# Kernel tuning notes

Hardware: AMD Instinct MI355X
Metric: run time of the kernel (lower is better)

Reference implementation:

```python
import jax, jax.numpy as jnp
import numpy as np

B, L, H, U = 4, 1024, 16, 64  # batch, length, num_heads, units (per-head dim)
D_IN = 1024                   # input feature dim
D_MODEL = H * U               # 1024


def setup_inputs() -> dict:
    key = jax.random.key(0)
    ks = jax.random.split(key, 12)
    s_in = 1.0 / np.sqrt(D_IN)
    s_md = 1.0 / np.sqrt(D_MODEL)
    return {
        "v": jax.random.normal(ks[0], (B, L, D_IN), jnp.float32),
        "k": jax.random.normal(ks[1], (B, L, D_IN), jnp.float32),
        "q": jax.random.normal(ks[2], (B, L, D_IN), jnp.float32),
        "wq": jax.random.normal(ks[3], (D_IN, D_MODEL), jnp.float32) * s_in,
        "bq": jnp.zeros((D_MODEL,), jnp.float32),
        "wk": jax.random.normal(ks[4], (D_IN, D_MODEL), jnp.float32) * s_in,
        "bk": jnp.zeros((D_MODEL,), jnp.float32),
        "wv": jax.random.normal(ks[5], (D_IN, D_MODEL), jnp.float32) * s_in,
        "bv": jnp.zeros((D_MODEL,), jnp.float32),
        "wo": jax.random.normal(ks[6], (D_MODEL, U), jnp.float32) * s_md,  # dense: units*num_heads -> units
        "bo": jnp.zeros((U,), jnp.float32),
    }


def _split_heads(x):
    # (B, L, H*U) -> (B, H, L, U)
    return x.reshape(B, L, H, U).transpose(0, 2, 1, 3)


def reference(v, k, q, wq, bq, wk, bk, wv, bv, wo, bo):
    qh = _split_heads(q @ wq + bq)
    kh = _split_heads(k @ wk + bk)
    vh = _split_heads(v @ wv + bv)
    scale = 1.0 / jnp.sqrt(jnp.asarray(U, jnp.float32))
    logits = jnp.einsum("bhqd,bhkd->bhqk", qh, kh) * scale
    attn = jax.nn.softmax(logits, axis=-1)  # (B, H, Lq, Lk)
    ctx = jnp.einsum("bhqk,bhkd->bhqd", attn, vh)
    concat = ctx.transpose(0, 2, 1, 3).reshape(B, L, D_MODEL)
    out = concat @ wo + bo  # (B, L, U)
    return out, attn
```

## Files before the change

### kernel.cpp

```cpp
#include <hip/hip_runtime.h>
#include <hip/hip_bf16.h>


typedef __attribute__((ext_vector_type(8))) short s8v;
typedef __attribute__((ext_vector_type(4))) float f4v;

#define MFMA16(a, b, c) __builtin_amdgcn_mfma_f32_16x16x32_bf16(a, b, c, 0, 0, 0)

__device__ __forceinline__ ushort f2bf(float x) {
    unsigned u = __float_as_uint(x);
    return (ushort)((u + 0x7FFF + ((u >> 16) & 1)) >> 16);
}
__device__ __forceinline__ void split2(float x, ushort& h, ushort& l) {
    h = f2bf(x);
    float hf = __uint_as_float(((unsigned)h) << 16);
    l = f2bf(x - hf);
}

__global__ __launch_bounds__(256) void pack_wt(const float* __restrict__ W,
                                               ushort* __restrict__ Wt_hi,
                                               ushort* __restrict__ Wt_lo) {
    __shared__ float tile[32][36];
    const int t = threadIdx.x;
    const int n0 = blockIdx.x * 32, k0 = blockIdx.y * 32;
    {
        const int kr = t >> 3, c4 = (t & 7) * 4;
        float4 v = *(const float4*)&W[(size_t)(k0 + kr) * 1024 + n0 + c4];
        *(float4*)&tile[kr][c4] = v;
    }
    __syncthreads();
    {
        const int n = t >> 3, k4 = (t & 7) * 4;
        ushort4 h, l;
        split2(tile[k4 + 0][n], h.x, l.x);
        split2(tile[k4 + 1][n], h.y, l.y);
        split2(tile[k4 + 2][n], h.z, l.z);
        split2(tile[k4 + 3][n], h.w, l.w);
        *(ushort4*)&Wt_hi[(size_t)(n0 + n) * 1024 + k0 + k4] = h;
        *(ushort4*)&Wt_lo[(size_t)(n0 + n) * 1024 + k0 + k4] = l;
    }
}

#define PROJ_LDSTRIDE 40
template <bool SPLIT>
__global__ __launch_bounds__(256, 2) void gemm_proj_mfma(
    const float* __restrict__ X, const ushort* __restrict__ Wt_hi,
    const ushort* __restrict__ Wt_lo, const float* __restrict__ bias,
    ushort* __restrict__ Yhi, ushort* __restrict__ Ylo) {
    __shared__ ushort As_hi[128 * PROJ_LDSTRIDE];
    __shared__ ushort As_lo[128 * PROJ_LDSTRIDE];
    __shared__ ushort Bs_hi[128 * PROJ_LDSTRIDE];
    __shared__ ushort Bs_lo[128 * PROJ_LDSTRIDE];

    const int t = threadIdx.x;
    const int lane = t & 63, w = t >> 6;
    const int wm = (w & 1) * 64, wn = (w >> 1) * 64;
    const int fr = lane & 15, q8 = (lane >> 4) * 8;
    const int row0 = blockIdx.y * 128, col0 = blockIdx.x * 128;

    const int srow = t >> 1, skb = (t & 1) * 16;

    f4v acc[4][4] = {};

    for (int k0 = 0; k0 < 1024; k0 += 32) {
        {
            const float* xp = &X[(size_t)(row0 + srow) * 1024 + k0 + skb];
#pragma unroll
            for (int j = 0; j < 4; ++j) {
                float4 x4 = *(const float4*)&xp[4 * j];
                ushort4 h, l;
                split2(x4.x, h.x, l.x);
                split2(x4.y, h.y, l.y);
                split2(x4.z, h.z, l.z);
                split2(x4.w, h.w, l.w);
                *(ushort4*)&As_hi[srow * PROJ_LDSTRIDE + skb + 4 * j] = h;
                if (SPLIT) *(ushort4*)&As_lo[srow * PROJ_LDSTRIDE + skb + 4 * j] = l;
            }
        }
        {
            const ushort* bp = &Wt_hi[(size_t)(col0 + srow) * 1024 + k0 + skb];
            *(uint4*)&Bs_hi[srow * PROJ_LDSTRIDE + skb] = *(const uint4*)bp;
            *(uint4*)&Bs_hi[srow * PROJ_LDSTRIDE + skb + 8] = *(const uint4*)(bp + 8);
            if (SPLIT) {
                const ushort* bl = &Wt_lo[(size_t)(col0 + srow) * 1024 + k0 + skb];
                *(uint4*)&Bs_lo[srow * PROJ_LDSTRIDE + skb] = *(const uint4*)bl;
                *(uint4*)&Bs_lo[srow * PROJ_LDSTRIDE + skb + 8] = *(const uint4*)(bl + 8);
            }
        }
        __syncthreads();

        s8v a_hi[4], a_lo[4], b_hi[4], b_lo[4];
#pragma unroll
        for (int mi = 0; mi < 4; ++mi) {
            a_hi[mi] = *(const s8v*)&As_hi[(wm + mi * 16 + fr) * PROJ_LDSTRIDE + q8];
            if (SPLIT) a_lo[mi] = *(const s8v*)&As_lo[(wm + mi * 16 + fr) * PROJ_LDSTRIDE + q8];
        }
#pragma unroll
        for (int ni = 0; ni < 4; ++ni) {
            b_hi[ni] = *(const s8v*)&Bs_hi[(wn + ni * 16 + fr) * PROJ_LDSTRIDE + q8];
            if (SPLIT) b_lo[ni] = *(const s8v*)&Bs_lo[(wn + ni * 16 + fr) * PROJ_LDSTRIDE + q8];
        }
#pragma unroll
        for (int mi = 0; mi < 4; ++mi)
#pragma unroll
            for (int ni = 0; ni < 4; ++ni) {
                acc[mi][ni] = MFMA16(a_hi[mi], b_hi[ni], acc[mi][ni]);
                if (SPLIT) {
                    acc[mi][ni] = MFMA16(a_hi[mi], b_lo[ni], acc[mi][ni]);
                    acc[mi][ni] = MFMA16(a_lo[mi], b_hi[ni], acc[mi][ni]);
                }
            }
        __syncthreads();
    }

#pragma unroll
    for (int mi = 0; mi < 4; ++mi)
#pragma unroll
        for (int ni = 0; ni < 4; ++ni)
#pragma unroll
            for (int r = 0; r < 4; ++r) {
                const int lr = wm + mi * 16 + (lane >> 4) * 4 + r;
                const int lc = wn + ni * 16 + fr;
                const int grow = row0 + lr;
                const int b = grow >> 10, ll = grow & 1023;
                const int gcol = col0 + lc;
                const int h = gcol >> 6, u = gcol & 63;
                const float val = acc[mi][ni][r] + bias[gcol];
                const size_t o = ((size_t)((b * 16 + h) * 1024 + ll)) * 64 + u;
                if (SPLIT) {
                    ushort hh, lll;
                    split2(val, hh, lll);
                    Yhi[o] = hh;
                    Ylo[o] = lll;
                } else {
                    Yhi[o] = f2bf(val);
                }
            }
}

__global__ __launch_bounds__(256) void trans_vh(const ushort* __restrict__ vh,
                                                ushort* __restrict__ vhT) {
    __shared__ ushort st[64][72];
    const int t = threadIdx.x;
    const int bh = blockIdx.y, l0 = blockIdx.x * 64;
    {
        const int l = t >> 2, uc = (t & 3) * 16;
        const ushort* src = &vh[((size_t)bh * 1024 + l0 + l) * 64 + uc];
        *(uint4*)&st[l][uc] = *(const uint4*)src;
        *(uint4*)&st[l][uc + 8] = *(const uint4*)(src + 8);
    }
    __syncthreads();
    {
        const int u = t >> 2, lc = (t & 3) * 16;
        ushort tmp[16];
#pragma unroll
        for (int i = 0; i < 16; ++i) tmp[i] = st[lc + i][u];
        ushort* dst = &vhT[((size_t)bh * 64 + u) * 1024 + l0 + lc];
        *(uint4*)dst = *(uint4*)&tmp[0];
        *(uint4*)(dst + 8) = *(uint4*)&tmp[8];
    }
}

__device__ __forceinline__ int pswz(int row, int b) {
    return row * 2048 + (b ^ ((row & 7) << 4) ^ ((row & 8) << 2));
}

__global__ __launch_bounds__(256, 4) void attn_fused(
    const ushort* __restrict__ qh_hi, const ushort* __restrict__ qh_lo,
    const ushort* __restrict__ kh_hi, const ushort* __restrict__ kh_lo,
    const ushort* __restrict__ vhT, float* __restrict__ attn,
    float* __restrict__ ctx) {
    __shared__ ushort Pl[16 * 1024];
    __shared__ float redA[4][16];
    __shared__ float redB[4][16];

    const int t = threadIdx.x, lane = t & 63, w = t >> 6;
    const int bid = blockIdx.x;
    const int sbid = (bid & 7) * 512 + (bid >> 3);
    const int bh = sbid >> 6, q0 = (sbid & 63) * 16;
    const int fr = lane & 15, g = lane >> 4, q8 = g * 8;
    const size_t hbase = (size_t)bh * 1024 * 64;

    const ushort* qp = &qh_hi[hbase + (size_t)(q0 + fr) * 64];
    const ushort* ql = &qh_lo[hbase + (size_t)(q0 + fr) * 64];
    const s8v qb_h0 = *(const s8v*)(qp + q8), qb_h1 = *(const s8v*)(qp + 32 + q8);
    const s8v qb_l0 = *(const s8v*)(ql + q8), qb_l1 = *(const s8v*)(ql + 32 + q8);

    f4v lg[16];
#pragma unroll
    for (int i = 0; i < 16; ++i) {
        const int nt = 2 * w + 8 * (i >> 1) + (i & 1);
        const ushort* kp = &kh_hi[hbase + (size_t)(nt * 16 + fr) * 64];
        const ushort* kl = &kh_lo[hbase + (size_t)(nt * 16 + fr) * 64];
        const s8v ka_h0 = *(const s8v*)(kp + q8), ka_h1 = *(const s8v*)(kp + 32 + q8);
        const s8v ka_l0 = *(const s8v*)(kl + q8), ka_l1 = *(const s8v*)(kl + 32 + q8);
        f4v a0 = {}, a1 = {}, a2 = {};
        a0 = MFMA16(ka_h0, qb_h0, a0);
        a0 = MFMA16(ka_h1, qb_h1, a0);
        a1 = MFMA16(ka_l0, qb_h0, a1);
        a1 = MFMA16(ka_l1, qb_h1, a1);
        a2 = MFMA16(ka_h0, qb_l0, a2);
        a2 = MFMA16(ka_h1, qb_l1, a2);
#pragma unroll
        for (int r = 0; r < 4; ++r) lg[i][r] = (a0[r] + a1[r] + a2[r]) * 0.125f;
    }

    f4v mv = lg[0];
#pragma unroll
    for (int i = 1; i < 16; ++i) {
#pragma unroll
        for (int r = 0; r < 4; ++r) mv[r] = fmaxf(mv[r], lg[i][r]);
    }
    float m = fmaxf(fmaxf(mv[0], mv[1]), fmaxf(mv[2], mv[3]));
    m = fmaxf(m, __shfl_xor(m, 16));
    m = fmaxf(m, __shfl_xor(m, 32));
    if (lane < 16) redA[w][lane] = m;
    __syncthreads();
    const float m4 = fmaxf(fmaxf(redA[0][fr], redA[1][fr]),
                           fmaxf(redA[2][fr], redA[3][fr]));

    f4v sv = {0.f, 0.f, 0.f, 0.f};
#pragma unroll
    for (int i = 0; i < 16; ++i) {
#pragma unroll
        for (int r = 0; r < 4; ++r) {
            const float e = __expf(lg[i][r] - m4);
            lg[i][r] = e;
            sv[r] += e;
        }
    }
    float s = (sv[0] + sv[1]) + (sv[2] + sv[3]);
    s += __shfl_xor(s, 16);
    s += __shfl_xor(s, 32);
    if (lane < 16) redB[w][lane] = s;
    __syncthreads();
    const float inv = 1.0f / (redB[0][fr] + redB[1][fr] + redB[2][fr] + redB[3][fr]);

    char* Pb = (char*)Pl;
    float* abase = attn + ((size_t)bh << 20) + (size_t)(q0 + fr) * 1024;
#pragma unroll
    for (int j = 0; j < 8; ++j) {
        const int ntA = 2 * w + 8 * j, ntB = ntA + 1;
        const int iA = 2 * j, iB = 2 * j + 1;
        const int colA = ntA * 16 + 4 * g, colB = ntB * 16 + 4 * g;
        float4 pA, pB;
        pA.x = lg[iA][0] * inv; pA.y = lg[iA][1] * inv;
        pA.z = lg[iA][2] * inv; pA.w = lg[iA][3] * inv;
        pB.x = lg[iB][0] * inv; pB.y = lg[iB][1] * inv;
        pB.z = lg[iB][2] * inv; pB.w = lg[iB][3] * inv;
        *(float4*)&abase[colA] = pA;
        *(float4*)&abase[colB] = pB;
        ushort4 bA, bB;
        bA.x = f2bf(pA.x); bA.y = f2bf(pA.y); bA.z = f2bf(pA.z); bA.w = f2bf(pA.w);
        bB.x = f2bf(pB.x); bB.y = f2bf(pB.y); bB.z = f2bf(pB.z); bB.w = f2bf(pB.w);
        *(ushort4*)(Pb + pswz(fr, colA * 2)) = bA;
        *(ushort4*)(Pb + pswz(fr, colB * 2)) = bB;
    }
    __syncthreads();

    f4v cacc = {};
    const ushort* vp = &vhT[hbase + (size_t)(w * 16 + fr) * 1024];
#pragma unroll 4
    for (int ks = 0; ks < 32; ++ks) {
        const s8v a = *(const s8v*)(Pb + pswz(fr, ks * 64 + q8 * 2));
        const s8v b = *(const s8v*)(vp + ks * 32 + q8);
        cacc = MFMA16(a, b, cacc);
    }
#pragma unroll
    for (int r = 0; r < 4; ++r)
        ctx[((size_t)bh * 1024 + q0 + 4 * g + r) * 64 + w * 16 + fr] = cacc[r];
}

#define LDS_PAD 68
__global__ __launch_bounds__(256) void gemm_out(const float* __restrict__ ctx,
                                                const float* __restrict__ wo,
                                                const float* __restrict__ bo,
                                                float* __restrict__ out) {
    __shared__ float As[16][LDS_PAD];
    __shared__ float Bs[16][LDS_PAD];
    const int t = threadIdx.x;
    const int tx = t & 15, ty = t >> 4;
    const int row0 = blockIdx.y * 64;

    const int am = t >> 2, ak4 = t & 3;
    const int bk = t >> 4, bn4 = t & 15;

    float acc[4][4] = {};
    for (int k0 = 0; k0 < 1024; k0 += 16) {
        const int r = row0 + am;
        const int b = r >> 10, l = r & 1023;
        const int c = k0 + ak4 * 4;
        const int h = c >> 6, d = c & 63;
        float4 a = *(const float4*)&ctx[(size_t)((b * 16 + h) * 1024 + l) * 64 + d];
        float4 bvv = *(const float4*)&wo[(size_t)(k0 + bk) * 64 + bn4 * 4];
        As[ak4 * 4 + 0][am] = a.x; As[ak4 * 4 + 1][am] = a.y;
        As[ak4 * 4 + 2][am] = a.z; As[ak4 * 4 + 3][am] = a.w;
        Bs[bk][bn4 * 4 + 0] = bvv.x; Bs[bk][bn4 * 4 + 1] = bvv.y;
        Bs[bk][bn4 * 4 + 2] = bvv.z; Bs[bk][bn4 * 4 + 3] = bvv.w;
        __syncthreads();
#pragma unroll
        for (int kk = 0; kk < 16; ++kk) {
            float av[4], bv[4];
#pragma unroll
            for (int i = 0; i < 4; ++i) av[i] = As[kk][ty * 4 + i];
#pragma unroll
            for (int j = 0; j < 4; ++j) bv[j] = Bs[kk][tx * 4 + j];
#pragma unroll
            for (int i = 0; i < 4; ++i)
#pragma unroll
                for (int j = 0; j < 4; ++j) acc[i][j] += av[i] * bv[j];
        }
        __syncthreads();
    }
#pragma unroll
    for (int i = 0; i < 4; ++i) {
        const int r = row0 + ty * 4 + i;
#pragma unroll
        for (int j = 0; j < 4; ++j) {
            const int u = tx * 4 + j;
            out[(size_t)r * 64 + u] = acc[i][j] + bo[u];
        }
    }
}

extern "C" void kernel_launch(void* const* d_in, const int* in_sizes, int n_in,
                              void* d_out, int out_size, void* d_ws, size_t ws_size,
                              hipStream_t stream) {
    const float* v_in = (const float*)d_in[0];
    const float* k_in = (const float*)d_in[1];
    const float* q_in = (const float*)d_in[2];
    const float* wq = (const float*)d_in[3];
    const float* bq = (const float*)d_in[4];
    const float* wk = (const float*)d_in[5];
    const float* bk = (const float*)d_in[6];
    const float* wv = (const float*)d_in[7];
    const float* bv = (const float*)d_in[8];
    const float* wo = (const float*)d_in[9];
    const float* bo = (const float*)d_in[10];

    float* out = (float*)d_out;
    float* attn = out + 262144;

    char* w8 = (char*)d_ws;
    const size_t MB = 1u << 20;
    ushort* wtq_hi = (ushort*)(w8 + 0 * MB);
    ushort* wtq_lo = (ushort*)(w8 + 2 * MB);
    ushort* wtk_hi = (ushort*)(w8 + 4 * MB);
    ushort* wtk_lo = (ushort*)(w8 + 6 * MB);
    ushort* wtv_hi = (ushort*)(w8 + 8 * MB);
    ushort* wtv_lo = (ushort*)(w8 + 10 * MB);
    ushort* qh_hi = (ushort*)(w8 + 12 * MB);
    ushort* qh_lo = (ushort*)(w8 + 20 * MB);
    ushort* kh_hi = (ushort*)(w8 + 28 * MB);
    ushort* kh_lo = (ushort*)(w8 + 36 * MB);
    ushort* vh_hi = (ushort*)(w8 + 44 * MB);
    ushort* vh_lo = (ushort*)(w8 + 52 * MB);
    ushort* vhT = (ushort*)(w8 + 60 * MB);
    float* ctx = (float*)(w8 + 68 * MB);

    dim3 blk(256);
    pack_wt<<<dim3(32, 32), blk, 0, stream>>>(wq, wtq_hi, wtq_lo);
    pack_wt<<<dim3(32, 32), blk, 0, stream>>>(wk, wtk_hi, wtk_lo);
    pack_wt<<<dim3(32, 32), blk, 0, stream>>>(wv, wtv_hi, wtv_lo);

    gemm_proj_mfma<true><<<dim3(8, 32), blk, 0, stream>>>(q_in, wtq_hi, wtq_lo, bq, qh_hi, qh_lo);
    gemm_proj_mfma<true><<<dim3(8, 32), blk, 0, stream>>>(k_in, wtk_hi, wtk_lo, bk, kh_hi, kh_lo);
    gemm_proj_mfma<false><<<dim3(8, 32), blk, 0, stream>>>(v_in, wtv_hi, wtv_lo, bv, vh_hi, vh_lo);

    trans_vh<<<dim3(16, 64), blk, 0, stream>>>(vh_hi, vhT);

    attn_fused<<<dim3(4096), blk, 0, stream>>>(qh_hi, qh_lo, kh_hi, kh_lo, vhT, attn, ctx);

    gemm_out<<<dim3(1, 64), blk, 0, stream>>>(ctx, wo, bo, out);
}
```

Before: 735.0 us.

## Enlarge attention block to 64 query rows with 16 waves

The fused attention kernel now uses 1024-thread blocks that each handle 64 query rows. Sixteen waves are arranged as a 4x4 grid of query groups by key groups, and the grid shrinks from 4096 blocks to 1024. Each wave still computes 16 key tiles, but they are now contiguous, and the bf16 probability tile in LDS grows to 128 KB. The aim is to reuse K and V loads across more query rows per block, at the cost of much higher LDS use per block, which limits how many blocks can be resident per CU, and __launch_bounds__(1024,4) may force register spills.

```diff
diff --git a/kernel.cpp b/kernel.cpp
--- a/kernel.cpp
+++ b/kernel.cpp
@@ -165,31 +165,33 @@
     return row * 2048 + (b ^ ((row & 7) << 4) ^ ((row & 8) << 2));
 }
 
-__global__ __launch_bounds__(256, 4) void attn_fused(
+__global__ __launch_bounds__(1024, 4) void attn_fused(
     const ushort* __restrict__ qh_hi, const ushort* __restrict__ qh_lo,
     const ushort* __restrict__ kh_hi, const ushort* __restrict__ kh_lo,
     const ushort* __restrict__ vhT, float* __restrict__ attn,
     float* __restrict__ ctx) {
-    __shared__ ushort Pl[16 * 1024];
-    __shared__ float redA[4][16];
-    __shared__ float redB[4][16];
+    __shared__ ushort Pl[64 * 1024];
+    __shared__ float redA[4][4][16];
+    __shared__ float redB[4][4][16];
 
     const int t = threadIdx.x, lane = t & 63, w = t >> 6;
+    const int qi = w >> 2, ki = w & 3;
     const int bid = blockIdx.x;
-    const int sbid = (bid & 7) * 512 + (bid >> 3);
-    const int bh = sbid >> 6, q0 = (sbid & 63) * 16;
+    const int sbid = (bid & 7) * 128 + (bid >> 3);
+    const int bh = sbid >> 4, q0 = (sbid & 15) * 64;
     const int fr = lane & 15, g = lane >> 4, q8 = g * 8;
     const size_t hbase = (size_t)bh * 1024 * 64;
-
-    const ushort* qp = &qh_hi[hbase + (size_t)(q0 + fr) * 64];
-    const ushort* ql = &qh_lo[hbase + (size_t)(q0 + fr) * 64];
+    const int qrow = q0 + 16 * qi + fr;
+
+    const ushort* qp = &qh_hi[hbase + (size_t)qrow * 64];
+    const ushort* ql = &qh_lo[hbase + (size_t)qrow * 64];
     const s8v qb_h0 = *(const s8v*)(qp + q8), qb_h1 = *(const s8v*)(qp + 32 + q8);
     const s8v qb_l0 = *(const s8v*)(ql + q8), qb_l1 = *(const s8v*)(ql + 32 + q8);
 
     f4v lg[16];
 #pragma unroll
     for (int i = 0; i < 16; ++i) {
-        const int nt = 2 * w + 8 * (i >> 1) + (i & 1);
+        const int nt = 16 * ki + i;
         const ushort* kp = &kh_hi[hbase + (size_t)(nt * 16 + fr) * 64];
         const ushort* kl = &kh_lo[hbase + (size_t)(nt * 16 + fr) * 64];
         const s8v ka_h0 = *(const s8v*)(kp + q8), ka_h1 = *(const s8v*)(kp + 32 + q8);
@@ -214,10 +216,10 @@
     float m = fmaxf(fmaxf(mv[0], mv[1]), fmaxf(mv[2], mv[3]));
     m = fmaxf(m, __shfl_xor(m, 16));
     m = fmaxf(m, __shfl_xor(m, 32));
-    if (lane < 16) redA[w][lane] = m;
-    __syncthreads();
-    const float m4 = fmaxf(fmaxf(redA[0][fr], redA[1][fr]),
-                           fmaxf(redA[2][fr], redA[3][fr]));
+    if (lane < 16) redA[ki][qi][lane] = m;
+    __syncthreads();
+    const float m4 = fmaxf(fmaxf(redA[0][qi][fr], redA[1][qi][fr]),
+                           fmaxf(redA[2][qi][fr], redA[3][qi][fr]));
 
     f4v sv = {0.f, 0.f, 0.f, 0.f};
 #pragma unroll
@@ -232,17 +234,19 @@
     float s = (sv[0] + sv[1]) + (sv[2] + sv[3]);
     s += __shfl_xor(s, 16);
     s += __shfl_xor(s, 32);
-    if (lane < 16) redB[w][lane] = s;
-    __syncthreads();
-    const float inv = 1.0f / (redB[0][fr] + redB[1][fr] + redB[2][fr] + redB[3][fr]);
+    if (lane < 16) redB[ki][qi][lane] = s;
+    __syncthreads();
+    const float inv =
+        1.0f / (redB[0][qi][fr] + redB[1][qi][fr] + redB[2][qi][fr] + redB[3][qi][fr]);
 
     char* Pb = (char*)Pl;
-    float* abase = attn + ((size_t)bh << 20) + (size_t)(q0 + fr) * 1024;
+    const int prow = 16 * qi + fr;
+    float* abase = attn + ((size_t)bh << 20) + (size_t)qrow * 1024;
 #pragma unroll
     for (int j = 0; j < 8; ++j) {
-        const int ntA = 2 * w + 8 * j, ntB = ntA + 1;
         const int iA = 2 * j, iB = 2 * j + 1;
-        const int colA = ntA * 16 + 4 * g, colB = ntB * 16 + 4 * g;
+        const int ntA = 16 * ki + iA;
+        const int colA = ntA * 16 + 4 * g, colB = colA + 16;
         float4 pA, pB;
         pA.x = lg[iA][0] * inv; pA.y = lg[iA][1] * inv;
         pA.z = lg[iA][2] * inv; pA.w = lg[iA][3] * inv;
@@ -253,22 +257,24 @@
         ushort4 bA, bB;
         bA.x = f2bf(pA.x); bA.y = f2bf(pA.y); bA.z = f2bf(pA.z); bA.w = f2bf(pA.w);
         bB.x = f2bf(pB.x); bB.y = f2bf(pB.y); bB.z = f2bf(pB.z); bB.w = f2bf(pB.w);
-        *(ushort4*)(Pb + pswz(fr, colA * 2)) = bA;
-        *(ushort4*)(Pb + pswz(fr, colB * 2)) = bB;
-    }
-    __syncthreads();
-
+        *(ushort4*)(Pb + pswz(prow, colA * 2)) = bA;
+        *(ushort4*)(Pb + pswz(prow, colB * 2)) = bB;
+    }
+    __syncthreads();
+
+    const int ui = ki;
     f4v cacc = {};
-    const ushort* vp = &vhT[hbase + (size_t)(w * 16 + fr) * 1024];
+    const ushort* vp = &vhT[hbase + (size_t)(ui * 16 + fr) * 1024];
 #pragma unroll 4
     for (int ks = 0; ks < 32; ++ks) {
-        const s8v a = *(const s8v*)(Pb + pswz(fr, ks * 64 + q8 * 2));
+        const s8v a = *(const s8v*)(Pb + pswz(prow, ks * 64 + q8 * 2));
         const s8v b = *(const s8v*)(vp + ks * 32 + q8);
         cacc = MFMA16(a, b, cacc);
     }
 #pragma unroll
     for (int r = 0; r < 4; ++r)
-        ctx[((size_t)bh * 1024 + q0 + 4 * g + r) * 64 + w * 16 + fr] = cacc[r];
+        ctx[((size_t)bh * 1024 + q0 + 16 * qi + 4 * g + r) * 64 + ui * 16 + fr] =
+            cacc[r];
 }
 
 #define LDS_PAD 68
@@ -369,7 +375,7 @@
 
     trans_vh<<<dim3(16, 64), blk, 0, stream>>>(vh_hi, vhT);
 
-    attn_fused<<<dim3(4096), blk, 0, stream>>>(qh_hi, qh_lo, kh_hi, kh_lo, vhT, attn, ctx);
+    attn_fused<<<dim3(1024), dim3(1024), 0, stream>>>(qh_hi, qh_lo, kh_hi, kh_lo, vhT, attn, ctx);
 
     gemm_out<<<dim3(1, 64), blk, 0, stream>>>(ctx, wo, bo, out);
 }
```

Measured after the change: 781.5 us. 6.3% more time.
